# Kernel tuning notes

Measured on AMD Instinct MI355X. Metric: run time of the kernel, lower is better.

Reference implementation:

```python
import jax, jax.numpy as jnp
import numpy as np

N_NODES = 100000
N_EDGES = 3200000
HIDDEN = 64


def _gcn_conv(x, W, b, row, col, norm, n_nodes):
    # x: [N, Fin] -> [N, Fout]; symmetric-normalized scatter-add aggregation
    xw = x @ W  # [N, Fout]
    msg = xw[row] * norm[:, None]  # [E', Fout] gather + scale
    out = jax.ops.segment_sum(msg, col, num_segments=n_nodes)  # scatter-add
    return out + b


def _norm_and_loops(edge_index, n_nodes):
    # add self loops (PyG GCNConv default) and compute D^-1/2 norm per edge
    loops = jnp.arange(n_nodes, dtype=edge_index.dtype)
    row = jnp.concatenate([edge_index[0], loops])
    col = jnp.concatenate([edge_index[1], loops])
    deg = jax.ops.segment_sum(jnp.ones_like(col, dtype=jnp.float32), col,
                              num_segments=n_nodes)
    dis = jnp.where(deg > 0, 1.0 / jnp.sqrt(deg), 0.0)
    norm = dis[row] * dis[col]
    return row, col, norm


def setup_inputs() -> dict:
    key = jax.random.key(0)
    k1, k2, k3, k4 = jax.random.split(key, 4)
    x = jax.random.normal(k1, (N_NODES, 1), dtype=jnp.float32)
    edge_index = jax.random.randint(k2, (2, N_EDGES), 0, N_NODES, dtype=jnp.int64)
    # Glorot-ish init for GCN weights
    W1 = jax.random.normal(k3, (1, HIDDEN), dtype=jnp.float32) * (1.0 / np.sqrt(1))
    b1 = jnp.zeros((HIDDEN,), dtype=jnp.float32)
    W2 = jax.random.normal(k4, (HIDDEN, 1), dtype=jnp.float32) * (1.0 / np.sqrt(HIDDEN))
    b2 = jnp.zeros((1,), dtype=jnp.float32)
    return {"x": x, "edge_index": edge_index, "W1": W1, "b1": b1, "W2": W2, "b2": b2}


def reference(x, edge_index, W1, b1, W2, b2):
    n = x.shape[0]
    row, col, norm = _norm_and_loops(edge_index, n)
    h = _gcn_conv(x, W1, b1, row, col, norm, n)   # [N, 64]
    out = _gcn_conv(h, W2, b2, row, col, norm, n)  # [N, 1]
    return out
```

## Files before the change

### kernel.cpp

```cpp
#include <hip/hip_runtime.h>
#include <math.h>


#define CHUNK 256
#define CHUNK_SHIFT 8
#define PACK_SHIFT 17
#define ROW_MASK ((1u << PACK_SHIFT) - 1u)
#define NBMAX 512
#define TPB 512
#define PLACE_GRID 256
#define PLACE_TPB 1024

static __device__ __forceinline__ int gid() {
    return blockIdx.x * blockDim.x + threadIdx.x;
}

__global__ void __launch_bounds__(PLACE_TPB)
k_place(const int* __restrict__ row, const int* __restrict__ col,
        int E, int NB, int CAP, int* __restrict__ cursor,
        unsigned* __restrict__ sorted) {
    __shared__ int cnt[NBMAX];
    __shared__ int bbase[NBMAX];
    const int tid = threadIdx.x;
    int quads = E >> 2;
    int per = (quads + gridDim.x - 1) / gridDim.x;
    int qlo = blockIdx.x * per;
    int qhi = min(quads, qlo + per);

    for (int t = tid; t < NB; t += PLACE_TPB) cnt[t] = 0;
    __syncthreads();
    for (int q = qlo + tid; q < qhi; q += PLACE_TPB) {
        int4 c = reinterpret_cast<const int4*>(col)[q];
        atomicAdd(&cnt[c.x >> CHUNK_SHIFT], 1);
        atomicAdd(&cnt[c.y >> CHUNK_SHIFT], 1);
        atomicAdd(&cnt[c.z >> CHUNK_SHIFT], 1);
        atomicAdd(&cnt[c.w >> CHUNK_SHIFT], 1);
    }
    __syncthreads();
    for (int t = tid; t < NB; t += PLACE_TPB) {
        int c = cnt[t];
        bbase[t] = c ? atomicAdd(&cursor[t], c) : 0;
        cnt[t] = 0;
    }
    __syncthreads();
    for (int q = qlo + tid; q < qhi; q += PLACE_TPB) {
        int4 r = reinterpret_cast<const int4*>(row)[q];
        int4 c = reinterpret_cast<const int4*>(col)[q];
        {
            int b = c.x >> CHUNK_SHIFT;
            int off = bbase[b] + atomicAdd(&cnt[b], 1);
            if (off < CAP)
                sorted[(size_t)b * CAP + off] =
                    (unsigned)r.x | ((unsigned)(c.x & (CHUNK - 1)) << PACK_SHIFT);
        }
        {
            int b = c.y >> CHUNK_SHIFT;
            int off = bbase[b] + atomicAdd(&cnt[b], 1);
            if (off < CAP)
                sorted[(size_t)b * CAP + off] =
                    (unsigned)r.y | ((unsigned)(c.y & (CHUNK - 1)) << PACK_SHIFT);
        }
        {
            int b = c.z >> CHUNK_SHIFT;
            int off = bbase[b] + atomicAdd(&cnt[b], 1);
            if (off < CAP)
                sorted[(size_t)b * CAP + off] =
                    (unsigned)r.z | ((unsigned)(c.z & (CHUNK - 1)) << PACK_SHIFT);
        }
        {
            int b = c.w >> CHUNK_SHIFT;
            int off = bbase[b] + atomicAdd(&cnt[b], 1);
            if (off < CAP)
                sorted[(size_t)b * CAP + off] =
                    (unsigned)r.w | ((unsigned)(c.w & (CHUNK - 1)) << PACK_SHIFT);
        }
    }
    if (blockIdx.x == 0 && tid == 0) {
        for (int j = quads << 2; j < E; ++j) {
            int cc = col[j];
            int b = cc >> CHUNK_SHIFT;
            int off = atomicAdd(&cursor[b], 1);
            if (off < CAP)
                sorted[(size_t)b * CAP + off] =
                    (unsigned)row[j] | ((unsigned)(cc & (CHUNK - 1)) << PACK_SHIFT);
        }
    }
}


__global__ void __launch_bounds__(TPB)
k_acc1(const unsigned* __restrict__ sorted, const int* __restrict__ cursor, int CAP,
       const float* __restrict__ x, float* __restrict__ dis, float* __restrict__ g,
       int N) {
    __shared__ float acc[CHUNK];
    const int b = blockIdx.x;
    const int tid = threadIdx.x;
    if (tid < CHUNK) acc[tid] = 0.0f;
    __syncthreads();
    int len = min(cursor[b], CAP);
    const unsigned* bs = sorted + (size_t)b * CAP;
    int quads = len >> 2;
    for (int j = tid; j < quads; j += TPB) {
        uint4 p = reinterpret_cast<const uint4*>(bs)[j];
        atomicAdd(&acc[p.x >> PACK_SHIFT], 1.0f);
        atomicAdd(&acc[p.y >> PACK_SHIFT], 1.0f);
        atomicAdd(&acc[p.z >> PACK_SHIFT], 1.0f);
        atomicAdd(&acc[p.w >> PACK_SHIFT], 1.0f);
    }
    if (tid < (len & 3))
        atomicAdd(&acc[bs[(quads << 2) + tid] >> PACK_SHIFT], 1.0f);
    __syncthreads();
    int i = b * CHUNK + tid;
    if (tid < CHUNK && i < N) {
        float d = rsqrtf(1.0f + acc[tid]);
        dis[i] = d;
        g[i] = d * x[i];
    }
}

__global__ void __launch_bounds__(TPB)
k_acc2(const unsigned* __restrict__ sorted, const int* __restrict__ cursor, int CAP,
       const float* __restrict__ g, const float* __restrict__ dis,
       const float* __restrict__ W1, const float* __restrict__ b1,
       const float* __restrict__ W2, int H,
       float* __restrict__ g2, int N) {
    __shared__ float acc[CHUNK];
    __shared__ float sab[2];
    const int b = blockIdx.x;
    const int tid = threadIdx.x;
    if (tid < CHUNK) acc[tid] = 0.0f;
    if (tid < 64) {
        float w2 = (tid < H) ? W2[tid] : 0.0f;
        float a = (tid < H) ? W1[tid] * w2 : 0.0f;
        float bb = (tid < H) ? b1[tid] * w2 : 0.0f;
        for (int o = 32; o; o >>= 1) {
            a += __shfl_down(a, o, 64);
            bb += __shfl_down(bb, o, 64);
        }
        if (tid == 0) { sab[0] = a; sab[1] = bb; }
    }
    __syncthreads();
    int len = min(cursor[b], CAP);
    const unsigned* bs = sorted + (size_t)b * CAP;
    int quads = len >> 2;
    for (int j = tid; j < quads; j += TPB) {
        uint4 p = reinterpret_cast<const uint4*>(bs)[j];
        float vx = g[p.x & ROW_MASK];
        float vy = g[p.y & ROW_MASK];
        float vz = g[p.z & ROW_MASK];
        float vw = g[p.w & ROW_MASK];
        atomicAdd(&acc[p.x >> PACK_SHIFT], vx);
        atomicAdd(&acc[p.y >> PACK_SHIFT], vy);
        atomicAdd(&acc[p.z >> PACK_SHIFT], vz);
        atomicAdd(&acc[p.w >> PACK_SHIFT], vw);
    }
    if (tid < (len & 3)) {
        unsigned p = bs[(quads << 2) + tid];
        atomicAdd(&acc[p >> PACK_SHIFT], g[p & ROW_MASK]);
    }
    __syncthreads();
    int i = b * CHUNK + tid;
    if (tid < CHUNK && i < N) {
        float d = dis[i];
        float s = d * (g[i] + acc[tid]);
        g2[i] = d * (sab[0] * s + sab[1]);
    }
}

__global__ void __launch_bounds__(TPB)
k_acc3(const unsigned* __restrict__ sorted, const int* __restrict__ cursor, int CAP,
       const float* __restrict__ g2, const float* __restrict__ dis,
       const float* __restrict__ b2, float* __restrict__ out, int N) {
    __shared__ float acc[CHUNK];
    const int b = blockIdx.x;
    const int tid = threadIdx.x;
    if (tid < CHUNK) acc[tid] = 0.0f;
    __syncthreads();
    int len = min(cursor[b], CAP);
    const unsigned* bs = sorted + (size_t)b * CAP;
    int quads = len >> 2;
    for (int j = tid; j < quads; j += TPB) {
        uint4 p = reinterpret_cast<const uint4*>(bs)[j];
        float vx = g2[p.x & ROW_MASK];
        float vy = g2[p.y & ROW_MASK];
        float vz = g2[p.z & ROW_MASK];
        float vw = g2[p.w & ROW_MASK];
        atomicAdd(&acc[p.x >> PACK_SHIFT], vx);
        atomicAdd(&acc[p.y >> PACK_SHIFT], vy);
        atomicAdd(&acc[p.z >> PACK_SHIFT], vz);
        atomicAdd(&acc[p.w >> PACK_SHIFT], vw);
    }
    if (tid < (len & 3)) {
        unsigned p = bs[(quads << 2) + tid];
        atomicAdd(&acc[p >> PACK_SHIFT], g2[p & ROW_MASK]);
    }
    __syncthreads();
    int i = b * CHUNK + tid;
    if (tid < CHUNK && i < N)
        out[i] = dis[i] * (g2[i] + acc[tid]) + b2[0];
}


__global__ void k_zero_f(float* __restrict__ p, int n) {
    int i = gid();
    if (i < n) p[i] = 0.0f;
}

__global__ void k_ab_fb(const float* __restrict__ W1, const float* __restrict__ b1,
                        const float* __restrict__ W2, float* __restrict__ ab, int hidden) {
    int t = threadIdx.x;
    float w2 = (t < hidden) ? W2[t] : 0.0f;
    float a = (t < hidden) ? W1[t] * w2 : 0.0f;
    float b = (t < hidden) ? b1[t] * w2 : 0.0f;
    for (int o = 32; o; o >>= 1) {
        a += __shfl_down(a, o, 64);
        b += __shfl_down(b, o, 64);
    }
    if (t == 0) { ab[0] = a; ab[1] = b; }
}

__global__ void k_deg_fb(const int* __restrict__ col, float* __restrict__ t, int E) {
    int i = gid();
    if (i < E) atomicAdd(&t[col[i]], 1.0f);
}

__global__ void k_scat_fb(const int* __restrict__ ei, const float* __restrict__ val,
                          float* __restrict__ t, int E) {
    int i = gid();
    if (i < E) atomicAdd(&t[ei[E + i]], val[ei[i]]);
}

__global__ void k_node1_fb(const float* __restrict__ x, const float* __restrict__ degsum,
                           float* __restrict__ dis, float* __restrict__ g, int N) {
    int i = gid();
    if (i < N) {
        float d = rsqrtf(1.0f + degsum[i]);
        dis[i] = d;
        g[i] = d * x[i];
    }
}

__global__ void k_node2_fb(const float* __restrict__ g, const float* __restrict__ dis,
                           const float* __restrict__ ab, const float* __restrict__ sum1,
                           float* __restrict__ g2, int N) {
    int i = gid();
    if (i < N) {
        float s = dis[i] * (g[i] + sum1[i]);
        g2[i] = dis[i] * (ab[0] * s + ab[1]);
    }
}

__global__ void k_node3_fb(const float* __restrict__ g2, const float* __restrict__ dis,
                           const float* __restrict__ b2, const float* __restrict__ sum2,
                           float* __restrict__ out, int N) {
    int i = gid();
    if (i < N) out[i] = dis[i] * (g2[i] + sum2[i]) + b2[0];
}

extern "C" void kernel_launch(void* const* d_in, const int* in_sizes, int n_in,
                              void* d_out, int out_size, void* d_ws, size_t ws_size,
                              hipStream_t stream) {
    const float* x  = (const float*)d_in[0];
    const int*   ei = (const int*)d_in[1];
    const float* W1 = (const float*)d_in[2];
    const float* b1 = (const float*)d_in[3];
    const float* W2 = (const float*)d_in[4];
    const float* b2 = (const float*)d_in[5];
    float* out = (float*)d_out;

    const int N = in_sizes[0];
    const int E = in_sizes[1] / 2;
    const int H = in_sizes[2];
    const int NB = (N + CHUNK - 1) >> CHUNK_SHIFT;

    int mean = (E + NB - 1) / NB;
    int CAP = mean + (mean >> 3) + 512;
    CAP = (CAP + 255) & ~255;

    char* w = (char*)d_ws;
    unsigned* sorted = (unsigned*)w;   w += (size_t)NB * CAP * 4;
    float* dis = (float*)w;            w += (size_t)N * 4;
    float* g   = (float*)w;            w += (size_t)N * 4;
    float* g2  = (float*)w;            w += (size_t)N * 4;
    int* cursor = (int*)w;             w += NBMAX * 4;
    size_t needed = (size_t)(w - (char*)d_ws);

    const int BLK = 256;
    const int nodeGrid = (N + BLK - 1) / BLK;

    if (N <= (1 << PACK_SHIFT) && NB <= NBMAX && H <= 64 && ws_size >= needed) {
        hipMemsetAsync(cursor, 0, NBMAX * 4, stream);
        k_place<<<PLACE_GRID, PLACE_TPB, 0, stream>>>(ei, ei + E, E, NB, CAP, cursor, sorted);
        k_acc1<<<NB, TPB, 0, stream>>>(sorted, cursor, CAP, x, dis, g, N);
        k_acc2<<<NB, TPB, 0, stream>>>(sorted, cursor, CAP, g, dis, W1, b1, W2, H, g2, N);
        k_acc3<<<NB, TPB, 0, stream>>>(sorted, cursor, CAP, g2, dis, b2, out, N);
    } else {
        float* fdis = (float*)d_ws;
        float* fg   = fdis + N;
        float* fg2  = fg + N;
        float* ftmp = fg2 + N;
        float* fab  = ftmp + N;
        const int eGrid = (E + BLK - 1) / BLK;
        k_ab_fb<<<1, 64, 0, stream>>>(W1, b1, W2, fab, H);
        k_zero_f<<<nodeGrid, BLK, 0, stream>>>(ftmp, N);
        k_deg_fb<<<eGrid, BLK, 0, stream>>>(ei + E, ftmp, E);
        k_node1_fb<<<nodeGrid, BLK, 0, stream>>>(x, ftmp, fdis, fg, N);
        k_zero_f<<<nodeGrid, BLK, 0, stream>>>(ftmp, N);
        k_scat_fb<<<eGrid, BLK, 0, stream>>>(ei, fg, ftmp, E);
        k_node2_fb<<<nodeGrid, BLK, 0, stream>>>(fg, fdis, fab, ftmp, fg2, N);
        k_zero_f<<<nodeGrid, BLK, 0, stream>>>(ftmp, N);
        k_scat_fb<<<eGrid, BLK, 0, stream>>>(ei, fg2, ftmp, E);
        k_node3_fb<<<nodeGrid, BLK, 0, stream>>>(fg2, fdis, b2, ftmp, out, N);
    }
}
```

Baseline: 105.1 us.

## Stage bucketed edges in shared memory before coalesced global scatter

Result: faster. 100.9 us (-4.0%).

```diff
diff --git a/kernel.cpp b/kernel.cpp
--- a/kernel.cpp
+++ b/kernel.cpp
@@ -7,9 +7,10 @@
 #define PACK_SHIFT 17
 #define ROW_MASK ((1u << PACK_SHIFT) - 1u)
 #define NBMAX 512
+#define SLICES 256
 #define TPB 512
-#define PLACE_GRID 256
 #define PLACE_TPB 1024
+#define STAGE_CAP 12544
 
 static __device__ __forceinline__ int gid() {
     return blockIdx.x * blockDim.x + threadIdx.x;
@@ -19,16 +20,20 @@
 k_place(const int* __restrict__ row, const int* __restrict__ col,
         int E, int NB, int CAP, int* __restrict__ cursor,
         unsigned* __restrict__ sorted) {
+    __shared__ unsigned stage[STAGE_CAP];
     __shared__ int cnt[NBMAX];
-    __shared__ int bbase[NBMAX];
+    __shared__ int soff[NBMAX];
+    __shared__ int wcnt[NBMAX];
+    __shared__ int gbase[NBMAX];
     const int tid = threadIdx.x;
+    const int blk = blockIdx.x;
     int quads = E >> 2;
     int per = (quads + gridDim.x - 1) / gridDim.x;
-    int qlo = blockIdx.x * per;
-    int qhi = min(quads, qlo + per);
-
-    for (int t = tid; t < NB; t += PLACE_TPB) cnt[t] = 0;
-    __syncthreads();
+    int qlo = blk * per, qhi = min(quads, qlo + per);
+
+    for (int t = tid; t < NBMAX; t += PLACE_TPB) { cnt[t] = 0; wcnt[t] = 0; }
+    __syncthreads();
+
     for (int q = qlo + tid; q < qhi; q += PLACE_TPB) {
         int4 c = reinterpret_cast<const int4*>(col)[q];
         atomicAdd(&cnt[c.x >> CHUNK_SHIFT], 1);
@@ -36,54 +41,73 @@
         atomicAdd(&cnt[c.z >> CHUNK_SHIFT], 1);
         atomicAdd(&cnt[c.w >> CHUNK_SHIFT], 1);
     }
-    __syncthreads();
-    for (int t = tid; t < NB; t += PLACE_TPB) {
-        int c = cnt[t];
-        bbase[t] = c ? atomicAdd(&cursor[t], c) : 0;
-        cnt[t] = 0;
-    }
-    __syncthreads();
+    if (blk == 0 && tid == 0)
+        for (int j = quads << 2; j < E; ++j)
+            atomicAdd(&cnt[col[j] >> CHUNK_SHIFT], 1);
+    __syncthreads();
+
+    if (tid < NBMAX) soff[tid] = cnt[tid];
+    __syncthreads();
+    for (int o = 1; o < NBMAX; o <<= 1) {
+        int v = 0;
+        if (tid < NBMAX) {
+            v = soff[tid];
+            if (tid >= o) v += soff[tid - o];
+        }
+        __syncthreads();
+        if (tid < NBMAX) soff[tid] = v;
+        __syncthreads();
+    }
+    if (tid < NBMAX) soff[tid] -= cnt[tid];
+    if (tid < NB) {
+        int c = cnt[tid];
+        gbase[tid] = c ? atomicAdd(&cursor[tid], c) : 0;
+    }
+    __syncthreads();
+
     for (int q = qlo + tid; q < qhi; q += PLACE_TPB) {
         int4 r = reinterpret_cast<const int4*>(row)[q];
         int4 c = reinterpret_cast<const int4*>(col)[q];
         {
             int b = c.x >> CHUNK_SHIFT;
-            int off = bbase[b] + atomicAdd(&cnt[b], 1);
-            if (off < CAP)
-                sorted[(size_t)b * CAP + off] =
-                    (unsigned)r.x | ((unsigned)(c.x & (CHUNK - 1)) << PACK_SHIFT);
+            int p = soff[b] + atomicAdd(&wcnt[b], 1);
+            stage[p] = (unsigned)r.x | ((unsigned)(c.x & (CHUNK - 1)) << PACK_SHIFT);
         }
         {
             int b = c.y >> CHUNK_SHIFT;
-            int off = bbase[b] + atomicAdd(&cnt[b], 1);
-            if (off < CAP)
-                sorted[(size_t)b * CAP + off] =
-                    (unsigned)r.y | ((unsigned)(c.y & (CHUNK - 1)) << PACK_SHIFT);
+            int p = soff[b] + atomicAdd(&wcnt[b], 1);
+            stage[p] = (unsigned)r.y | ((unsigned)(c.y & (CHUNK - 1)) << PACK_SHIFT);
         }
         {
             int b = c.z >> CHUNK_SHIFT;
-            int off = bbase[b] + atomicAdd(&cnt[b], 1);
-            if (off < CAP)
-                sorted[(size_t)b * CAP + off] =
-                    (unsigned)r.z | ((unsigned)(c.z & (CHUNK - 1)) << PACK_SHIFT);
+            int p = soff[b] + atomicAdd(&wcnt[b], 1);
+            stage[p] = (unsigned)r.z | ((unsigned)(c.z & (CHUNK - 1)) << PACK_SHIFT);
         }
         {
             int b = c.w >> CHUNK_SHIFT;
-            int off = bbase[b] + atomicAdd(&cnt[b], 1);
-            if (off < CAP)
-                sorted[(size_t)b * CAP + off] =
-                    (unsigned)r.w | ((unsigned)(c.w & (CHUNK - 1)) << PACK_SHIFT);
-        }
-    }
-    if (blockIdx.x == 0 && tid == 0) {
+            int p = soff[b] + atomicAdd(&wcnt[b], 1);
+            stage[p] = (unsigned)r.w | ((unsigned)(c.w & (CHUNK - 1)) << PACK_SHIFT);
+        }
+    }
+    if (blk == 0 && tid == 0) {
         for (int j = quads << 2; j < E; ++j) {
             int cc = col[j];
             int b = cc >> CHUNK_SHIFT;
-            int off = atomicAdd(&cursor[b], 1);
-            if (off < CAP)
-                sorted[(size_t)b * CAP + off] =
-                    (unsigned)row[j] | ((unsigned)(cc & (CHUNK - 1)) << PACK_SHIFT);
-        }
+            int p = soff[b] + atomicAdd(&wcnt[b], 1);
+            stage[p] = (unsigned)row[j] | ((unsigned)(cc & (CHUNK - 1)) << PACK_SHIFT);
+        }
+    }
+    __syncthreads();
+
+    const int wid = tid >> 6, lane = tid & 63;
+    const int nw = PLACE_TPB >> 6;
+    for (int b = wid; b < NB; b += nw) {
+        int c = cnt[b];
+        int gb = gbase[b];
+        if (gb + c > CAP) c = max(0, CAP - gb);
+        int lb = soff[b];
+        unsigned* dst = sorted + (size_t)b * CAP + gb;
+        for (int i = lane; i < c; i += 64) dst[i] = stage[lb + i];
     }
 }
 
@@ -99,9 +123,10 @@
     __syncthreads();
     int len = min(cursor[b], CAP);
     const unsigned* bs = sorted + (size_t)b * CAP;
+    const uint4* bs4 = reinterpret_cast<const uint4*>(bs);
     int quads = len >> 2;
     for (int j = tid; j < quads; j += TPB) {
-        uint4 p = reinterpret_cast<const uint4*>(bs)[j];
+        uint4 p = bs4[j];
         atomicAdd(&acc[p.x >> PACK_SHIFT], 1.0f);
         atomicAdd(&acc[p.y >> PACK_SHIFT], 1.0f);
         atomicAdd(&acc[p.z >> PACK_SHIFT], 1.0f);
@@ -129,22 +154,24 @@
     const int b = blockIdx.x;
     const int tid = threadIdx.x;
     if (tid < CHUNK) acc[tid] = 0.0f;
-    if (tid < 64) {
-        float w2 = (tid < H) ? W2[tid] : 0.0f;
-        float a = (tid < H) ? W1[tid] * w2 : 0.0f;
-        float bb = (tid < H) ? b1[tid] * w2 : 0.0f;
+    if (tid >= CHUNK && tid < CHUNK + 64) {
+        int t = tid - CHUNK;
+        float w2 = (t < H) ? W2[t] : 0.0f;
+        float a = (t < H) ? W1[t] * w2 : 0.0f;
+        float bb = (t < H) ? b1[t] * w2 : 0.0f;
         for (int o = 32; o; o >>= 1) {
             a += __shfl_down(a, o, 64);
             bb += __shfl_down(bb, o, 64);
         }
-        if (tid == 0) { sab[0] = a; sab[1] = bb; }
+        if (t == 0) { sab[0] = a; sab[1] = bb; }
     }
     __syncthreads();
     int len = min(cursor[b], CAP);
     const unsigned* bs = sorted + (size_t)b * CAP;
+    const uint4* bs4 = reinterpret_cast<const uint4*>(bs);
     int quads = len >> 2;
     for (int j = tid; j < quads; j += TPB) {
-        uint4 p = reinterpret_cast<const uint4*>(bs)[j];
+        uint4 p = bs4[j];
         float vx = g[p.x & ROW_MASK];
         float vy = g[p.y & ROW_MASK];
         float vz = g[p.z & ROW_MASK];
@@ -178,9 +205,10 @@
     __syncthreads();
     int len = min(cursor[b], CAP);
     const unsigned* bs = sorted + (size_t)b * CAP;
+    const uint4* bs4 = reinterpret_cast<const uint4*>(bs);
     int quads = len >> 2;
     for (int j = tid; j < quads; j += TPB) {
-        uint4 p = reinterpret_cast<const uint4*>(bs)[j];
+        uint4 p = bs4[j];
         float vx = g2[p.x & ROW_MASK];
         float vy = g2[p.y & ROW_MASK];
         float vz = g2[p.z & ROW_MASK];
@@ -273,24 +301,28 @@
     const int H = in_sizes[2];
     const int NB = (N + CHUNK - 1) >> CHUNK_SHIFT;
 
+    const int per_quads = ((E >> 2) + SLICES - 1) / SLICES;
+    const int stage_need = per_quads * 4 + 8;
+
     int mean = (E + NB - 1) / NB;
-    int CAP = mean + (mean >> 3) + 512;
+    int CAP = mean + 1024 + (mean >> 4);
     CAP = (CAP + 255) & ~255;
 
     char* w = (char*)d_ws;
     unsigned* sorted = (unsigned*)w;   w += (size_t)NB * CAP * 4;
+    int* cursor = (int*)w;             w += NBMAX * 4;
     float* dis = (float*)w;            w += (size_t)N * 4;
     float* g   = (float*)w;            w += (size_t)N * 4;
     float* g2  = (float*)w;            w += (size_t)N * 4;
-    int* cursor = (int*)w;             w += NBMAX * 4;
     size_t needed = (size_t)(w - (char*)d_ws);
 
     const int BLK = 256;
     const int nodeGrid = (N + BLK - 1) / BLK;
 
-    if (N <= (1 << PACK_SHIFT) && NB <= NBMAX && H <= 64 && ws_size >= needed) {
+    if (N <= (1 << PACK_SHIFT) && NB <= NBMAX && H <= 64 &&
+        stage_need <= STAGE_CAP && ws_size >= needed) {
         hipMemsetAsync(cursor, 0, NBMAX * 4, stream);
-        k_place<<<PLACE_GRID, PLACE_TPB, 0, stream>>>(ei, ei + E, E, NB, CAP, cursor, sorted);
+        k_place<<<SLICES, PLACE_TPB, 0, stream>>>(ei, ei + E, E, NB, CAP, cursor, sorted);
         k_acc1<<<NB, TPB, 0, stream>>>(sorted, cursor, CAP, x, dis, g, N);
         k_acc2<<<NB, TPB, 0, stream>>>(sorted, cursor, CAP, g, dis, W1, b1, W2, H, g2, N);
         k_acc3<<<NB, TPB, 0, stream>>>(sorted, cursor, CAP, g2, dis, b2, out, N);
```
